# Kernel optimization log

Measured on AMD Instinct MI355X. Metric: run time of the kernel, lower is better.

Reference implementation:

```python
import jax, jax.numpy as jnp
import numpy as np

D = 512           # embedding_dim
K = 4096          # num_embeddings
COMMITMENT_COST = 0.25


def setup_inputs() -> dict:
    key = jax.random.key(0)
    k1, k2 = jax.random.split(key)
    x = jax.random.normal(k1, (32, 32, 32, D), dtype=jnp.float32)
    # glorot-normal-ish init for the [D, K] codebook
    emb = jax.random.normal(k2, (D, K), dtype=jnp.float32) * np.float32(np.sqrt(2.0 / (D + K)))
    return {"x": x, "embeddings": emb}


def reference(x, embeddings):
    # x: [B, H, W, D]; embeddings: [D, K]
    flat = x.reshape(-1, D)  # [N, D]
    n = flat.shape[0]
    distances = (jnp.sum(flat * flat, axis=1, keepdims=True)
                 - 2.0 * (flat @ embeddings)
                 + jnp.sum(embeddings * embeddings, axis=0, keepdims=True))
    encoding_indices = jnp.argmin(distances, axis=1)  # [N]
    quantized = jnp.take(embeddings.T, encoding_indices, axis=0).reshape(x.shape)

    e_latent_loss = jnp.mean((jax.lax.stop_gradient(quantized) - x) ** 2)
    q_latent_loss = jnp.mean((quantized - jax.lax.stop_gradient(x)) ** 2)
    loss = q_latent_loss + COMMITMENT_COST * e_latent_loss

    # straight-through estimator
    quantized_st = x + jax.lax.stop_gradient(quantized - x)

    # perplexity without materializing the [N, K] one-hot
    avg_probs = jnp.zeros((K,), dtype=x.dtype).at[encoding_indices].add(1.0) / n
    perplexity = jnp.exp(-jnp.sum(avg_probs * jnp.log(avg_probs + 1e-10)))

    return quantized_st, loss, perplexity
```

## Files before the change

kernel.cpp:

```cpp
#include <hip/hip_runtime.h>
#include <stdint.h>

#define DD 512
#define KK 4096
#define NN 32768

typedef __attribute__((ext_vector_type(8))) short bf16x8;
typedef __attribute__((ext_vector_type(4))) float f32x4;

__device__ __forceinline__ unsigned short bf16_rn(float f) {
  uint32_t u = __float_as_uint(f);
  return (unsigned short)((u + 0x7FFFu + ((u >> 16) & 1u)) >> 16);
}

__device__ __forceinline__ float bf16_to_f32(unsigned short h) {
  return __uint_as_float((uint32_t)h << 16);
}

__global__ __launch_bounds__(256) void prep_fused_kernel(
    const float4* __restrict__ x4, unsigned short* __restrict__ xh,
    const float* __restrict__ E, unsigned short* __restrict__ Eth,
    float* __restrict__ he2) {
  __shared__ float t[32][33];
  const int bid = blockIdx.x;
  if (bid < 2048) {
    int bk = (bid & 127) * 32;
    int bd = (bid >> 7) * 32;
    int c = threadIdx.x & 31;
    int r0 = threadIdx.x >> 5;
#pragma unroll
    for (int r = r0; r < 32; r += 8) t[r][c] = E[(size_t)(bd + r) * KK + bk + c];
    __syncthreads();
#pragma unroll
    for (int i = 0; i < 4; ++i) {
      int r = r0 + i * 8;
      float v = t[c][r];
      Eth[(size_t)(bk + r) * DD + bd + c] = bf16_rn(v);
      float v2 = v * v;
#pragma unroll
      for (int m = 1; m < 32; m <<= 1) v2 += __shfl_xor(v2, m, 64);
      if (c == 0) atomicAdd(&he2[bk + r], 0.5f * v2);
    }
  } else {
    int gid = (bid - 2048) * 256 + threadIdx.x;
    float4 a = x4[gid * 2];
    float4 b = x4[gid * 2 + 1];
    union { unsigned short u[8]; uint4 q; } H;
    H.u[0] = bf16_rn(a.x); H.u[1] = bf16_rn(a.y);
    H.u[2] = bf16_rn(a.z); H.u[3] = bf16_rn(a.w);
    H.u[4] = bf16_rn(b.x); H.u[5] = bf16_rn(b.y);
    H.u[6] = bf16_rn(b.z); H.u[7] = bf16_rn(b.w);
    *(uint4*)(xh + (size_t)gid * 8) = H.q;
  }
}

#define ANB 512
#define BN 128
#define BMT 256

__device__ __forceinline__ void stage_tile2(const unsigned short* __restrict__ xh,
                                            const unsigned short* __restrict__ Eth,
                                            char* Ah, char* Bh, int block_m, int ncode,
                                            int dt, int w, int srow, int schunk) {
  const int col = dt + schunk * 8;
#pragma unroll
  for (int r = 0; r < 4; ++r) {
    const int rowbase = w * 32 + r * 8;
    const int arow = block_m + rowbase + srow;
    __builtin_amdgcn_global_load_lds(
        (const __attribute__((address_space(1))) void*)(xh + (size_t)arow * DD + col),
        (__attribute__((address_space(3))) void*)(Ah + rowbase * 128), 16, 0, 0);
  }
#pragma unroll
  for (int r = 0; r < 2; ++r) {
    const int rowbase = w * 16 + r * 8;
    const int brow = ncode + rowbase + srow;
    __builtin_amdgcn_global_load_lds(
        (const __attribute__((address_space(1))) void*)(Eth + (size_t)brow * DD + col),
        (__attribute__((address_space(3))) void*)(Bh + rowbase * 128), 16, 0, 0);
  }
}

__global__ __launch_bounds__(512, 2) void argmax_mfma_kernel(
    const unsigned short* __restrict__ xh, const unsigned short* __restrict__ Eth,
    const float* __restrict__ he2, unsigned long long* __restrict__ best64) {
  __shared__ __align__(16) char smem[98304];

  const int tid = threadIdx.x;
  const int w = tid >> 6;
  const int lane = tid & 63;
  const int wm = w >> 1, wk = w & 1;
  const int l15 = lane & 15, quad = lane >> 4;

  const int orig = blockIdx.x;
  const int wgid = (orig & 7) * 128 + (orig >> 3);
  const int block_m = (wgid >> 3) * BMT;
  const int nbase = (wgid & 7) * ANB;

  const int srow = lane >> 3;
  const int schunk = (lane & 7) ^ (lane >> 3);
  const int rx = l15 & 7;

  float best[16];
  int bidx[16];
#pragma unroll
  for (int s = 0; s < 16; ++s) { best[s] = -INFINITY; bidx[s] = 0; }

  stage_tile2(xh, Eth, smem, smem + 32768, block_m, nbase, 0, w, srow, schunk);
  __syncthreads();
  int cur = 0;

  for (int nt = 0; nt < 4; ++nt) {
    const int ncode = nbase + nt * BN;
    f32x4 acc[4][4];
#pragma unroll
    for (int ti = 0; ti < 4; ++ti)
#pragma unroll
      for (int tj = 0; tj < 4; ++tj) acc[ti][tj] = (f32x4){0.f, 0.f, 0.f, 0.f};

    for (int dtI = 0; dtI < 8; ++dtI) {
      char* nAh = smem + (cur ^ 1) * 49152;
      if (dtI < 7) {
        stage_tile2(xh, Eth, nAh, nAh + 32768, block_m, ncode, (dtI + 1) * 64, w, srow,
                    schunk);
      } else if (nt < 3) {
        stage_tile2(xh, Eth, nAh, nAh + 32768, block_m, ncode + BN, 0, w, srow, schunk);
      }

      char* Ah = smem + cur * 49152;
      char* Bh = Ah + 32768;
#pragma unroll
      for (int s = 0; s < 2; ++s) {
        const int ch = ((s * 4 + quad) ^ rx) * 16;
        bf16x8 af[4], bfv[4];
#pragma unroll
        for (int t = 0; t < 4; ++t) {
          af[t] = *(const bf16x8*)(Ah + (wm * 64 + t * 16 + l15) * 128 + ch);
          bfv[t] = *(const bf16x8*)(Bh + (wk * 64 + t * 16 + l15) * 128 + ch);
        }
#pragma unroll
        for (int ti = 0; ti < 4; ++ti)
#pragma unroll
          for (int tj = 0; tj < 4; ++tj)
            acc[ti][tj] = __builtin_amdgcn_mfma_f32_16x16x32_bf16(af[ti], bfv[tj],
                                                                  acc[ti][tj], 0, 0, 0);
      }
      __syncthreads();
      cur ^= 1;
    }

    const int colb = ncode + wk * 64 + l15;
#pragma unroll
    for (int tj = 0; tj < 4; ++tj) {
      float h = he2[colb + tj * 16];
#pragma unroll
      for (int ti = 0; ti < 4; ++ti)
#pragma unroll
        for (int r = 0; r < 4; ++r) {
          float sc = acc[ti][tj][r] - h;
          int slot = ti * 4 + r;
          if (sc > best[slot]) { best[slot] = sc; bidx[slot] = colb + tj * 16; }
        }
    }
  }

#pragma unroll
  for (int slot = 0; slot < 16; ++slot) {
    float v = best[slot];
    int ii = bidx[slot];
#pragma unroll
    for (int m = 1; m < 16; m <<= 1) {
      float ov = __shfl_xor(v, m, 64);
      int oi = __shfl_xor(ii, m, 64);
      if (ov > v || (ov == v && oi < ii)) { v = ov; ii = oi; }
    }
    if (l15 == 0) {
      int row = block_m + wm * 64 + (slot >> 2) * 16 + quad * 4 + (slot & 3);
      uint32_t b = __float_as_uint(v);
      uint32_t mm = (b & 0x80000000u) ? ~b : (b | 0x80000000u);
      unsigned long long packed = ((unsigned long long)mm << 32) | (uint32_t)(~(uint32_t)ii);
      atomicMax(&best64[row], packed);
    }
  }
}

#define BM 128
#define BK 128
#define KS 4
#define KPB (KK / KS)
#define BD 32

__global__ __launch_bounds__(256, 4) void argmax_kernel(
    const float* __restrict__ x, const float* __restrict__ E,
    const float* __restrict__ he2, unsigned long long* __restrict__ best64) {
  __shared__ __align__(16) char smem[33280];
  float (*xs)[132] = (float (*)[132])smem;
  float (*es)[BK] = (float (*)[BK])(smem + 16896);

  const int tid = threadIdx.x;
  const int wave = tid >> 6;
  const int lane = tid & 63;
  const int wm = wave >> 1, wk = wave & 1;
  const int tm = lane >> 3, tk = lane & 7;
  const int block_m = (blockIdx.x >> 2) * BM;
  const int kbase = (blockIdx.x & 3) * KPB;

  float best[8];
  int bidx[8];
#pragma unroll
  for (int i = 0; i < 8; ++i) { best[i] = -INFINITY; bidx[i] = 0; }

  const int xtok = tid >> 3;
  const int xd4 = tid & 7;
  const int erow_lane = (lane >> 5);
  const int ecol = (lane & 31) * 4;

  for (int kt = 0; kt < KPB; kt += BK) {
    const int k0 = kbase + kt;
    float acc[8][8];
#pragma unroll
    for (int i = 0; i < 8; ++i)
#pragma unroll
      for (int j = 0; j < 8; ++j) acc[i][j] = 0.f;

    for (int dt = 0; dt < DD; dt += BD) {
      __syncthreads();
#pragma unroll
      for (int r = 0; r < 4; ++r) {
        int row = r * 8 + wave * 2;
        const float* gp = E + (size_t)(dt + row + erow_lane) * KK + k0 + ecol;
        __builtin_amdgcn_global_load_lds(
            (const __attribute__((address_space(1))) void*)gp,
            (__attribute__((address_space(3))) void*)&es[row][0], 16, 0, 0);
      }
#pragma unroll
      for (int r = 0; r < 4; ++r) {
        int tok = xtok + r * 32;
        float4 v = *(const float4*)(x + (size_t)(block_m + tok) * DD + dt + xd4 * 4);
        xs[xd4 * 4 + 0][tok] = v.x;
        xs[xd4 * 4 + 1][tok] = v.y;
        xs[xd4 * 4 + 2][tok] = v.z;
        xs[xd4 * 4 + 3][tok] = v.w;
      }
      __syncthreads();
#pragma unroll 4
      for (int d = 0; d < BD; ++d) {
        const float4 a0 = *(const float4*)&xs[d][wm * 64 + tm * 8];
        const float4 a1 = *(const float4*)&xs[d][wm * 64 + tm * 8 + 4];
        const float4 b0 = *(const float4*)&es[d][wk * 64 + tk * 8];
        const float4 b1 = *(const float4*)&es[d][wk * 64 + tk * 8 + 4];
        const float av[8] = {a0.x, a0.y, a0.z, a0.w, a1.x, a1.y, a1.z, a1.w};
        const float bv[8] = {b0.x, b0.y, b0.z, b0.w, b1.x, b1.y, b1.z, b1.w};
#pragma unroll
        for (int i = 0; i < 8; ++i)
#pragma unroll
          for (int j = 0; j < 8; ++j) acc[i][j] = fmaf(av[i], bv[j], acc[i][j]);
      }
    }
    const int kcol = k0 + wk * 64 + tk * 8;
    float4 h0 = *(const float4*)(he2 + kcol);
    float4 h1 = *(const float4*)(he2 + kcol + 4);
    const float hv[8] = {h0.x, h0.y, h0.z, h0.w, h1.x, h1.y, h1.z, h1.w};
#pragma unroll
    for (int i = 0; i < 8; ++i) {
#pragma unroll
      for (int j = 0; j < 8; ++j) {
        float s = acc[i][j] - hv[j];
        if (s > best[i]) { best[i] = s; bidx[i] = kcol + j; }
      }
    }
  }

  __syncthreads();
  float (*rv)[17] = (float (*)[17])smem;
  int (*ri)[17] = (int (*)[17])(smem + 8704);
#pragma unroll
  for (int i = 0; i < 8; ++i) {
    int tok = wm * 64 + tm * 8 + i;
    rv[tok][wk * 8 + tk] = best[i];
    ri[tok][wk * 8 + tk] = bidx[i];
  }
  __syncthreads();
  if (tid < BM) {
    float bv = rv[tid][0];
    int bi = ri[tid][0];
#pragma unroll
    for (int t = 1; t < 16; ++t) {
      float v = rv[tid][t];
      int ii = ri[tid][t];
      if (v > bv || (v == bv && ii < bi)) { bv = v; bi = ii; }
    }
    uint32_t b = __float_as_uint(bv);
    uint32_t m = (b & 0x80000000u) ? ~b : (b | 0x80000000u);
    unsigned long long packed = ((unsigned long long)m << 32) | (uint32_t)(~(uint32_t)bi);
    atomicMax(&best64[block_m + tid], packed);
  }
}

__global__ __launch_bounds__(256) void gather_eth_kernel(
    const float* __restrict__ x, const unsigned short* __restrict__ Eth,
    const unsigned long long* __restrict__ best64, float* __restrict__ out,
    float* __restrict__ partials, int* __restrict__ counts) {
  __shared__ float sh[256];
  int tid = threadIdx.x;
  int gid = blockIdx.x * 256 + tid;
  int n = gid >> 7;
  int d4 = gid & 127;
  int k = (int)(~(uint32_t)best64[n]);
  ushort4 qh = *(const ushort4*)(Eth + (size_t)k * DD + d4 * 4);
  float4 q;
  q.x = bf16_to_f32(qh.x);
  q.y = bf16_to_f32(qh.y);
  q.z = bf16_to_f32(qh.z);
  q.w = bf16_to_f32(qh.w);
  float4 xv = *(const float4*)(x + (size_t)n * DD + d4 * 4);
  *(float4*)(out + (size_t)n * DD + d4 * 4) = q;
  float dx0 = q.x - xv.x, dx1 = q.y - xv.y, dx2 = q.z - xv.z, dx3 = q.w - xv.w;
  sh[tid] = dx0 * dx0 + dx1 * dx1 + dx2 * dx2 + dx3 * dx3;
  if (d4 == 0) atomicAdd(&counts[k], 1);
  __syncthreads();
  for (int s = 128; s > 0; s >>= 1) {
    if (tid < s) sh[tid] += sh[tid + s];
    __syncthreads();
  }
  if (tid == 0) atomicAdd(&partials[blockIdx.x & 255], sh[0]);
}

__global__ __launch_bounds__(256) void gather_direct_kernel(
    const float* __restrict__ x, const float* __restrict__ E,
    const unsigned long long* __restrict__ best64, float* __restrict__ out,
    float* __restrict__ partials, int* __restrict__ counts) {
  __shared__ float sh[256];
  int tid = threadIdx.x;
  int gid = blockIdx.x * 256 + tid;
  int n = gid >> 7;
  int d4 = gid & 127;
  int k = (int)(~(uint32_t)best64[n]);
  float4 q;
  q.x = E[(size_t)(d4 * 4 + 0) * KK + k];
  q.y = E[(size_t)(d4 * 4 + 1) * KK + k];
  q.z = E[(size_t)(d4 * 4 + 2) * KK + k];
  q.w = E[(size_t)(d4 * 4 + 3) * KK + k];
  float4 xv = *(const float4*)(x + (size_t)n * DD + d4 * 4);
  *(float4*)(out + (size_t)n * DD + d4 * 4) = q;
  float dx0 = q.x - xv.x, dx1 = q.y - xv.y, dx2 = q.z - xv.z, dx3 = q.w - xv.w;
  sh[tid] = dx0 * dx0 + dx1 * dx1 + dx2 * dx2 + dx3 * dx3;
  if (d4 == 0) atomicAdd(&counts[k], 1);
  __syncthreads();
  for (int s = 128; s > 0; s >>= 1) {
    if (tid < s) sh[tid] += sh[tid + s];
    __syncthreads();
  }
  if (tid == 0) atomicAdd(&partials[blockIdx.x & 255], sh[0]);
}

__global__ __launch_bounds__(256) void finalize_kernel(
    const int* __restrict__ counts, const float* __restrict__ partials,
    float* __restrict__ out) {
  __shared__ float sh[256];
  int tid = threadIdx.x;
  float h = 0.f;
  for (int k = tid; k < KK; k += 256) {
    float p = (float)counts[k] * (1.0f / (float)NN);
    h += p * logf(p + 1e-10f);
  }
  sh[tid] = h;
  __syncthreads();
  for (int s = 128; s > 0; s >>= 1) {
    if (tid < s) sh[tid] += sh[tid + s];
    __syncthreads();
  }
  float H = sh[0];
  __syncthreads();
  sh[tid] = partials[tid];
  __syncthreads();
  for (int s = 128; s > 0; s >>= 1) {
    if (tid < s) sh[tid] += sh[tid + s];
    __syncthreads();
  }
  if (tid == 0) {
    float mse = sh[0] / (float)((size_t)NN * DD);
    out[(size_t)NN * DD] = 1.25f * mse;
    out[(size_t)NN * DD + 1] = expf(-H);
  }
}

extern "C" void kernel_launch(void* const* d_in, const int* in_sizes, int n_in,
                              void* d_out, int out_size, void* d_ws, size_t ws_size,
                              hipStream_t stream) {
  const float* x = (const float*)d_in[0];
  const float* E = (const float*)d_in[1];
  float* out = (float*)d_out;
  char* ws = (char*)d_ws;

  unsigned long long* best64 = (unsigned long long*)(ws + 0);
  float* he2 = (float*)(ws + 262144);
  int* counts = (int*)(ws + 278528);
  float* partials = (float*)(ws + 294912);
  unsigned short* Eth = (unsigned short*)(ws + 295936);
  const size_t NEED_MFMA = 4490240;

  hipMemsetAsync(ws, 0, 295936, stream);

  if (ws_size >= NEED_MFMA) {
    unsigned short* xh = (unsigned short*)d_out;

    prep_fused_kernel<<<2048 + 8192, 256, 0, stream>>>((const float4*)x, xh, E, Eth,
                                                       he2);
    argmax_mfma_kernel<<<(NN / BMT) * 8, 512, 0, stream>>>(xh, Eth, he2, best64);
    gather_eth_kernel<<<(NN * (DD / 4)) / 256, 256, 0, stream>>>(x, Eth, best64, out,
                                                                 partials, counts);
  } else {
    prep_fused_kernel<<<2048 + 8192, 256, 0, stream>>>(
        (const float4*)x, (unsigned short*)d_out, E, Eth, he2);
    argmax_kernel<<<(NN / BM) * KS, 256, 0, stream>>>(x, E, he2, best64);
    gather_direct_kernel<<<(NN * (DD / 4)) / 256, 256, 0, stream>>>(x, E, best64, out,
                                                                    partials, counts);
  }
  finalize_kernel<<<1, 256, 0, stream>>>(counts, partials, out);
}
```

Baseline: 314.5 us.

## Triple-buffer LDS tiles with two-ahead prefetch and partial vmcnt waits

Replaces the double-buffered nested loop with a flattened 32-step loop over three LDS buffers, prefetching two tiles ahead. Each step waits only on the older loads via s_waitcnt vmcnt(6) plus a raw barrier instead of a full __syncthreads drain. The aim is to hide global-to-LDS latency behind MFMA work. LDS per block rises to 144KB, which likely allows only one block per CU instead of two.

```diff
diff --git a/kernel.cpp b/kernel.cpp
--- a/kernel.cpp
+++ b/kernel.cpp
@@ -57,6 +57,7 @@
 #define ANB 512
 #define BN 128
 #define BMT 256
+#define BUFSZ 49152
 
 __device__ __forceinline__ void stage_tile2(const unsigned short* __restrict__ xh,
                                             const unsigned short* __restrict__ Eth,
@@ -84,7 +85,7 @@
 __global__ __launch_bounds__(512, 2) void argmax_mfma_kernel(
     const unsigned short* __restrict__ xh, const unsigned short* __restrict__ Eth,
     const float* __restrict__ he2, unsigned long long* __restrict__ best64) {
-  __shared__ __align__(16) char smem[98304];
+  __shared__ __align__(16) char smem[147456];
 
   const int tid = threadIdx.x;
   const int w = tid >> 6;
@@ -107,60 +108,80 @@
   for (int s = 0; s < 16; ++s) { best[s] = -INFINITY; bidx[s] = 0; }
 
   stage_tile2(xh, Eth, smem, smem + 32768, block_m, nbase, 0, w, srow, schunk);
-  __syncthreads();
-  int cur = 0;
-
-  for (int nt = 0; nt < 4; ++nt) {
-    const int ncode = nbase + nt * BN;
-    f32x4 acc[4][4];
-#pragma unroll
-    for (int ti = 0; ti < 4; ++ti)
-#pragma unroll
-      for (int tj = 0; tj < 4; ++tj) acc[ti][tj] = (f32x4){0.f, 0.f, 0.f, 0.f};
-
-    for (int dtI = 0; dtI < 8; ++dtI) {
-      char* nAh = smem + (cur ^ 1) * 49152;
-      if (dtI < 7) {
-        stage_tile2(xh, Eth, nAh, nAh + 32768, block_m, ncode, (dtI + 1) * 64, w, srow,
-                    schunk);
-      } else if (nt < 3) {
-        stage_tile2(xh, Eth, nAh, nAh + 32768, block_m, ncode + BN, 0, w, srow, schunk);
-      }
-
-      char* Ah = smem + cur * 49152;
-      char* Bh = Ah + 32768;
-#pragma unroll
-      for (int s = 0; s < 2; ++s) {
-        const int ch = ((s * 4 + quad) ^ rx) * 16;
-        bf16x8 af[4], bfv[4];
-#pragma unroll
-        for (int t = 0; t < 4; ++t) {
-          af[t] = *(const bf16x8*)(Ah + (wm * 64 + t * 16 + l15) * 128 + ch);
-          bfv[t] = *(const bf16x8*)(Bh + (wk * 64 + t * 16 + l15) * 128 + ch);
-        }
+  stage_tile2(xh, Eth, smem + BUFSZ, smem + BUFSZ + 32768, block_m, nbase, 64, w, srow,
+              schunk);
+  asm volatile("s_waitcnt vmcnt(6)" ::: "memory");
+  __builtin_amdgcn_s_barrier();
+  asm volatile("" ::: "memory");
+
+  f32x4 acc[4][4];
+#pragma unroll
+  for (int ti = 0; ti < 4; ++ti)
+#pragma unroll
+    for (int tj = 0; tj < 4; ++tj) acc[ti][tj] = (f32x4){0.f, 0.f, 0.f, 0.f};
+
+  int cbuf = 0;
+  int sbuf = 2;
+
+  for (int T = 0; T < 32; ++T) {
+    if (T + 2 < 32) {
+      const int T2 = T + 2;
+      const int ncode2 = nbase + (T2 >> 3) * BN;
+      const int dt2 = (T2 & 7) * 64;
+      char* S = smem + sbuf * BUFSZ;
+      stage_tile2(xh, Eth, S, S + 32768, block_m, ncode2, dt2, w, srow, schunk);
+    }
+
+    char* Ah = smem + cbuf * BUFSZ;
+    char* Bh = Ah + 32768;
+#pragma unroll
+    for (int s = 0; s < 2; ++s) {
+      const int ch = ((s * 4 + quad) ^ rx) * 16;
+      bf16x8 af[4], bfv[4];
+#pragma unroll
+      for (int t = 0; t < 4; ++t) {
+        af[t] = *(const bf16x8*)(Ah + (wm * 64 + t * 16 + l15) * 128 + ch);
+        bfv[t] = *(const bf16x8*)(Bh + (wk * 64 + t * 16 + l15) * 128 + ch);
+      }
+#pragma unroll
+      for (int ti = 0; ti < 4; ++ti)
+#pragma unroll
+        for (int tj = 0; tj < 4; ++tj)
+          acc[ti][tj] = __builtin_amdgcn_mfma_f32_16x16x32_bf16(af[ti], bfv[tj],
+                                                                acc[ti][tj], 0, 0, 0);
+    }
+
+    asm volatile("" ::: "memory");
+    if (T + 2 < 32) {
+      asm volatile("s_waitcnt vmcnt(6)" ::: "memory");
+    } else {
+      asm volatile("s_waitcnt vmcnt(0)" ::: "memory");
+    }
+    __builtin_amdgcn_s_barrier();
+    asm volatile("" ::: "memory");
+
+    cbuf = (cbuf == 2) ? 0 : cbuf + 1;
+    sbuf = (sbuf == 2) ? 0 : sbuf + 1;
+
+    if ((T & 7) == 7) {
+      const int nt = T >> 3;
+      const int colb = nbase + nt * BN + wk * 64 + l15;
+#pragma unroll
+      for (int tj = 0; tj < 4; ++tj) {
+        float h = he2[colb + tj * 16];
 #pragma unroll
         for (int ti = 0; ti < 4; ++ti)
 #pragma unroll
-          for (int tj = 0; tj < 4; ++tj)
-            acc[ti][tj] = __builtin_amdgcn_mfma_f32_16x16x32_bf16(af[ti], bfv[tj],
-                                                                  acc[ti][tj], 0, 0, 0);
-      }
-      __syncthreads();
-      cur ^= 1;
-    }
-
-    const int colb = ncode + wk * 64 + l15;
-#pragma unroll
-    for (int tj = 0; tj < 4; ++tj) {
-      float h = he2[colb + tj * 16];
+          for (int r = 0; r < 4; ++r) {
+            float sc = acc[ti][tj][r] - h;
+            int slot = ti * 4 + r;
+            if (sc > best[slot]) { best[slot] = sc; bidx[slot] = colb + tj * 16; }
+          }
+      }
 #pragma unroll
       for (int ti = 0; ti < 4; ++ti)
 #pragma unroll
-        for (int r = 0; r < 4; ++r) {
-          float sc = acc[ti][tj][r] - h;
-          int slot = ti * 4 + r;
-          if (sc > best[slot]) { best[slot] = sc; bidx[slot] = colb + tj * 16; }
-        }
+        for (int tj = 0; tj < 4; ++tj) acc[ti][tj] = (f32x4){0.f, 0.f, 0.f, 0.f};
     }
   }
 
```

After: 327.5 us. 4.1% more time.
